# Kernel optimization log

Hardware: AMD Instinct MI355X
Metric: run time of the kernel (lower is better)

Reference implementation:

```python
import jax, jax.numpy as jnp
import numpy as np

B, S, D, H = 4, 2048, 768, 12
DEPTH = D // H


def setup_inputs() -> dict:
    key = jax.random.key(0)
    ks = jax.random.split(key, 8)
    scale = 1.0 / np.sqrt(D)
    inp = {
        "q": jax.random.normal(ks[0], (B, S, D), jnp.float32),
        "k": jax.random.normal(ks[1], (B, S, D), jnp.float32),
        "v": jax.random.normal(ks[2], (B, S, D), jnp.float32),
        # additive mask: 1.0 at disallowed (future) positions, causal
        "mask": jnp.triu(jnp.ones((S, S), jnp.float32), k=1)[None, None, :, :],
        "wq": jax.random.normal(ks[3], (D, D), jnp.float32) * scale,
        "wk": jax.random.normal(ks[4], (D, D), jnp.float32) * scale,
        "wv": jax.random.normal(ks[5], (D, D), jnp.float32) * scale,
        "w_dense": jax.random.normal(ks[6], (D, D), jnp.float32) * scale,
        "b_dense": jnp.zeros((D,), jnp.float32),
    }
    return inp


def _split_heads(x):
    b, s, _ = x.shape
    return x.reshape(b, s, H, DEPTH).transpose(0, 2, 1, 3)  # [B,H,S,depth]


def reference(q, k, v, mask, wq, wk, wv, w_dense, b_dense):
    qh = _split_heads(q @ wq.T)
    kh = _split_heads(k @ wk.T)
    vh = _split_heads(v @ wv.T)
    scale = jnp.sqrt(jnp.float32(DEPTH))
    logits = jnp.einsum("bhqd,bhkd->bhqk", qh, kh) / scale  # [B,H,S,S]
    logits = logits + mask * -1e9
    attn = jax.nn.softmax(logits, axis=-1)
    out = jnp.einsum("bhqk,bhkd->bhqd", attn, vh)
    out = out.transpose(0, 2, 1, 3).reshape(q.shape[0], -1, D)
    return out @ w_dense.T + b_dense
```

## Files before the change

### kernel.cpp

```cpp
#include <hip/hip_runtime.h>

typedef __attribute__((ext_vector_type(8))) short short8;
typedef __attribute__((ext_vector_type(4))) float f32x4;
typedef __attribute__((ext_vector_type(4))) unsigned int uint4v;

static __device__ __forceinline__ unsigned pack2(float x, float y) {
  unsigned ux = __float_as_uint(x) + 0x8000u;
  unsigned uy = __float_as_uint(y) + 0x8000u;
  return __builtin_amdgcn_perm(uy, ux, 0x07060302u);
}
static __device__ __forceinline__ unsigned packt(float x, float y) {
  return __builtin_amdgcn_perm(__float_as_uint(y), __float_as_uint(x), 0x07060302u);
}

#define GLDS(g, l)                                                                     \
  __builtin_amdgcn_global_load_lds((const __attribute__((address_space(1))) void*)(g), \
                                   (__attribute__((address_space(3))) void*)(l), 16, 0, 0)

__global__ __launch_bounds__(256) void cvt_all(const float* __restrict__ q,
                                               const float* __restrict__ k,
                                               const float* __restrict__ v,
                                               const float* __restrict__ w0,
                                               const float* __restrict__ w1,
                                               const float* __restrict__ w2,
                                               const float* __restrict__ w3,
                                               unsigned short* __restrict__ oq,
                                               unsigned short* __restrict__ ok,
                                               unsigned short* __restrict__ ov,
                                               unsigned short* __restrict__ o0,
                                               unsigned short* __restrict__ o1,
                                               unsigned short* __restrict__ o2,
                                               unsigned short* __restrict__ o3) {
  const int bx = blockIdx.x;
  const float* s;
  unsigned short* d;
  long i;
  if (bx < 18432) {
    int seg = bx / 6144;
    s = seg == 0 ? q : seg == 1 ? k : v;
    d = seg == 0 ? oq : seg == 1 ? ok : ov;
    i = (long)(bx - seg * 6144) * 256 + threadIdx.x;
  } else {
    int t = bx - 18432;
    int seg = t / 576;
    s = seg == 0 ? w0 : seg == 1 ? w1 : seg == 2 ? w2 : w3;
    d = seg == 0 ? o0 : seg == 1 ? o1 : seg == 2 ? o2 : o3;
    i = (long)(t - seg * 576) * 256 + threadIdx.x;
  }
  float4 val = ((const float4*)s)[i];
  uint2 o;
  o.x = pack2(val.x, val.y);
  o.y = pack2(val.z, val.w);
  *(uint2*)(d + 4 * i) = o;
}

template <int MODE>
static __device__ __forceinline__ void proj_body(const unsigned short* __restrict__ A,
                                                 const unsigned short* __restrict__ W,
                                                 unsigned short* __restrict__ O, int m0,
                                                 int n0, unsigned short* buf) {
  constexpr int K = 768;
  const int tid = threadIdx.x, lane = tid & 63, wave = tid >> 6;
  const int ln = lane & 15, quad = lane >> 4;
  const int wm = (wave & 1) << 6, wn = (wave >> 1) << 6;

  const int o0 = tid << 4, o1 = 4096 + (tid << 4);
  const unsigned short* gA0 = A + (long)(m0 + (o0 >> 6)) * K + ((o0 >> 4) & 3) * 8;
  const unsigned short* gA1 = A + (long)(m0 + (o1 >> 6)) * K + ((o1 >> 4) & 3) * 8;
  const unsigned short* gW0 = W + (long)(n0 + (o0 >> 6)) * K + ((o0 >> 4) & 3) * 8;
  const unsigned short* gW1 = W + (long)(n0 + (o1 >> 6)) * K + ((o1 >> 4) & 3) * 8;

  GLDS(gA0, buf + (o0 >> 1));
  GLDS(gA1, buf + (o1 >> 1));
  GLDS(gW0, buf + 8192 + (o0 >> 1));
  GLDS(gW1, buf + 8192 + (o1 >> 1));

  f32x4 acc[4][4] = {};
  for (int t = 0; t < 24; t++) {
    const int cur = t & 1, nxt = cur ^ 1;
    const int k1 = (t + 1) << 5;
    __syncthreads();
    if (t < 23) {
      GLDS(gA0 + k1, buf + nxt * 4096 + (o0 >> 1));
      GLDS(gA1 + k1, buf + nxt * 4096 + (o1 >> 1));
      GLDS(gW0 + k1, buf + 8192 + nxt * 4096 + (o0 >> 1));
      GLDS(gW1 + k1, buf + 8192 + nxt * 4096 + (o1 >> 1));
    }
    const unsigned short* As = buf + cur * 4096;
    const unsigned short* Bs = buf + 8192 + cur * 4096;
    short8 af[4], bfr[4];
#pragma unroll
    for (int mi = 0; mi < 4; mi++)
      af[mi] = *(const short8*)(As + (wm + mi * 16 + ln) * 32 + quad * 8);
#pragma unroll
    for (int ni = 0; ni < 4; ni++)
      bfr[ni] = *(const short8*)(Bs + (wn + ni * 16 + ln) * 32 + quad * 8);
#pragma unroll
    for (int mi = 0; mi < 4; mi++)
#pragma unroll
      for (int ni = 0; ni < 4; ni++)
        acc[mi][ni] = (MODE == 0)
                          ? __builtin_amdgcn_mfma_f32_16x16x32_bf16(bfr[ni], af[mi],
                                                                    acc[mi][ni], 0, 0, 0)
                          : __builtin_amdgcn_mfma_f32_16x16x32_bf16(af[mi], bfr[ni],
                                                                    acc[mi][ni], 0, 0, 0);
  }

  unsigned short* Ts = buf;
  __syncthreads();
  if (MODE == 0) {
#pragma unroll
    for (int mi = 0; mi < 4; mi++)
#pragma unroll
      for (int ni = 0; ni < 4; ni++) {
        f32x4 v = acc[mi][ni];
        int s = wm + mi * 16 + ln;
        int n = wn + ni * 16 + quad * 4;
        uint2 w2;
        w2.x = pack2(v[0], v[1]);
        w2.y = pack2(v[2], v[3]);
        *(uint2*)(Ts + s * 136 + n) = w2;
      }
    __syncthreads();
    const int part = tid & 7, sg0 = tid >> 3;
#pragma unroll
    for (int p = 0; p < 8; p++) {
      int seg = sg0 + p * 32;
      int hh = seg >> 7, s = seg & 127;
      short8 val = *(const short8*)(Ts + s * 136 + hh * 64 + part * 8);
      int gs = m0 + s;
      int bb = gs >> 11, srow = gs & 2047;
      int head = (n0 >> 6) + hh;
      *(short8*)(O + (((long)(bb * 12 + head) * 2048 + srow) << 6) + part * 8) = val;
    }
  } else {
#pragma unroll
    for (int mi = 0; mi < 4; mi++)
#pragma unroll
      for (int ni = 0; ni < 4; ni++) {
        f32x4 v = acc[mi][ni];
        int d = wn + ni * 16 + ln;
        int s = wm + mi * 16 + quad * 4;
        uint2 w2;
        w2.x = pack2(v[0], v[1]);
        w2.y = pack2(v[2], v[3]);
        *(uint2*)(Ts + d * 136 + s) = w2;
      }
    __syncthreads();
    const int part = tid & 15, r0 = tid >> 4;
    const int bb = m0 >> 11, sbase = m0 & 2047;
#pragma unroll
    for (int p = 0; p < 8; p++) {
      int d = r0 + p * 16;
      short8 val = *(const short8*)(Ts + d * 136 + part * 8);
      int head = (n0 >> 6) + (d >> 6);
      int dl = d & 63;
      *(short8*)(O + ((long)(bb * 12 + head) * 64 + dl) * 2048 + sbase + part * 8) = val;
    }
  }
}

__global__ __launch_bounds__(256) void proj_all(
    const unsigned short* __restrict__ qb, const unsigned short* __restrict__ kb,
    const unsigned short* __restrict__ vb, const unsigned short* __restrict__ wq,
    const unsigned short* __restrict__ wk, const unsigned short* __restrict__ wv,
    unsigned short* __restrict__ qh, unsigned short* __restrict__ kh,
    unsigned short* __restrict__ vt) {
  __shared__ unsigned short buf[17408];
  const int bx = blockIdx.x;
  const int xcd = bx & 7;
  const int i = bx >> 3;
  const int op = i / 48, j = i % 48;
  const int m0 = ((j / 6) * 8 + xcd) << 7, n0 = (j % 6) << 7;
  if (op == 0)
    proj_body<0>(qb, wq, qh, m0, n0, buf);
  else if (op == 1)
    proj_body<0>(kb, wk, kh, m0, n0, buf);
  else
    proj_body<1>(vb, wv, vt, m0, n0, buf);
}

__global__ __launch_bounds__(256) void dense_gemm(const unsigned short* __restrict__ A,
                                                  const unsigned short* __restrict__ W,
                                                  const float* __restrict__ bias,
                                                  float* __restrict__ out) {
  constexpr int K = 768;
  __shared__ unsigned short buf[16384];
  const int bx = blockIdx.x;
  const int xcd = bx & 7;
  const int i = bx >> 3;
  const int m0 = ((i / 6) * 8 + xcd) << 7;
  const int n0 = (i % 6) << 7;

  const int tid = threadIdx.x, lane = tid & 63, wave = tid >> 6;
  const int ln = lane & 15, quad = lane >> 4;
  const int wm = (wave & 1) << 6, wn = (wave >> 1) << 6;

  const int o0 = tid << 4, o1 = 4096 + (tid << 4);
  const unsigned short* gA0 = A + (long)(m0 + (o0 >> 6)) * K + ((o0 >> 4) & 3) * 8;
  const unsigned short* gA1 = A + (long)(m0 + (o1 >> 6)) * K + ((o1 >> 4) & 3) * 8;
  const unsigned short* gW0 = W + (long)(n0 + (o0 >> 6)) * K + ((o0 >> 4) & 3) * 8;
  const unsigned short* gW1 = W + (long)(n0 + (o1 >> 6)) * K + ((o1 >> 4) & 3) * 8;

  GLDS(gA0, buf + (o0 >> 1));
  GLDS(gA1, buf + (o1 >> 1));
  GLDS(gW0, buf + 8192 + (o0 >> 1));
  GLDS(gW1, buf + 8192 + (o1 >> 1));

  f32x4 acc[4][4] = {};
  for (int t = 0; t < 24; t++) {
    const int cur = t & 1, nxt = cur ^ 1;
    const int k1 = (t + 1) << 5;
    __syncthreads();
    if (t < 23) {
      GLDS(gA0 + k1, buf + nxt * 4096 + (o0 >> 1));
      GLDS(gA1 + k1, buf + nxt * 4096 + (o1 >> 1));
      GLDS(gW0 + k1, buf + 8192 + nxt * 4096 + (o0 >> 1));
      GLDS(gW1 + k1, buf + 8192 + nxt * 4096 + (o1 >> 1));
    }
    const unsigned short* As = buf + cur * 4096;
    const unsigned short* Bs = buf + 8192 + cur * 4096;
    short8 af[4], bfr[4];
#pragma unroll
    for (int mi = 0; mi < 4; mi++)
      af[mi] = *(const short8*)(As + (wm + mi * 16 + ln) * 32 + quad * 8);
#pragma unroll
    for (int ni = 0; ni < 4; ni++)
      bfr[ni] = *(const short8*)(Bs + (wn + ni * 16 + ln) * 32 + quad * 8);
#pragma unroll
    for (int mi = 0; mi < 4; mi++)
#pragma unroll
      for (int ni = 0; ni < 4; ni++)
        acc[mi][ni] =
            __builtin_amdgcn_mfma_f32_16x16x32_bf16(bfr[ni], af[mi], acc[mi][ni], 0, 0, 0);
  }

#pragma unroll
  for (int mi = 0; mi < 4; mi++) {
    const int m = m0 + wm + mi * 16 + ln;
#pragma unroll
    for (int ni = 0; ni < 4; ni++) {
      const int n = n0 + wn + ni * 16 + quad * 4;
      f32x4 v = acc[mi][ni];
      float4 bv = *(const float4*)(bias + n);
      float4 st;
      st.x = v[0] + bv.x;
      st.y = v[1] + bv.y;
      st.z = v[2] + bv.z;
      st.w = v[3] + bv.w;
      *(float4*)(out + (long)m * 768 + n) = st;
    }
  }
}

__global__ __launch_bounds__(256, 3) void attn_kernel(const unsigned short* __restrict__ Qh,
                                                      const unsigned short* __restrict__ Kh,
                                                      const unsigned short* __restrict__ Vt,
                                                      unsigned short* __restrict__ outp) {
  constexpr int S = 2048;
  constexpr float CEXP = 0.18033688011112042f;
  __shared__ unsigned short sbuf[16384];

  const int bx = blockIdx.x;
  const int xcd = bx & 7;
  const int ii = bx >> 3;
  const int pr = ii & 15, grp = ii >> 4;
  const int bh = grp * 8 + xcd;
  const int h = bh % 12, b = bh / 12;
  const int qtA = pr, qtB = 31 - pr;
  const int tid = threadIdx.x, wave = tid >> 6, lane = tid & 63;
  const int ln = lane & 15, quad = lane >> 4;

  const unsigned short* Qg = Qh + (long)(b * 12 + h) * S * 64;
  const unsigned short* Kg = Kh + (long)(b * 12 + h) * S * 64;
  const unsigned short* Vg = Vt + (long)(b * 12 + h) * 64 * S;

  const int qrA = qtA * 64 + wave * 16 + ln;
  const int qrB = qtB * 64 + wave * 16 + ln;

  short8 bQa0 = *(const short8*)(Qg + qrA * 64 + quad * 8);
  short8 bQa1 = *(const short8*)(Qg + qrA * 64 + 32 + quad * 8);
  short8 bQb0 = *(const short8*)(Qg + qrB * 64 + quad * 8);
  short8 bQb1 = *(const short8*)(Qg + qrB * 64 + 32 + quad * 8);

  float sumA = 0.f, sumB = 0.f;
  f32x4 Oa[4] = {};
  f32x4 Ob[4] = {};
  unsigned pkA[8][2], pkB[8][2];

  const int nkA = (qtA >> 1) + 1;
  const int nkB = (qtB >> 1) + 1;
  const int l0 = ln + ((quad & 1) << 5);
  const bool hi = quad >= 2;

  const int srow = tid >> 2, sc = (tid & 3) << 3;
  const int koff0 = srow * 64 + sc;
  const int koff1 = (srow + 64) * 64 + sc;
  const int koff2 = srow * 64 + 32 + sc;
  const int koff3 = (srow + 64) * 64 + 32 + sc;
  const long voff = (long)srow * 2048 + sc;

  short8 kc[4], vc[4];
  {
    kc[0] = *(const short8*)(Kg + koff0);
    kc[1] = *(const short8*)(Kg + koff1);
    kc[2] = *(const short8*)(Kg + koff2);
    kc[3] = *(const short8*)(Kg + koff3);
    vc[0] = *(const short8*)(Vg + voff);
    vc[1] = *(const short8*)(Vg + voff + 32);
    vc[2] = *(const short8*)(Vg + voff + 64);
    vc[3] = *(const short8*)(Vg + voff + 96);
  }

  for (int kt = 0; kt < nkB; kt++) {
    __syncthreads();
    {
      unsigned short* w = sbuf + tid * 8;
      *(short8*)(w) = kc[0];
      *(short8*)(w + 2048) = kc[1];
      *(short8*)(w + 4096) = kc[2];
      *(short8*)(w + 6144) = kc[3];
      *(short8*)(w + 8192) = vc[0];
      *(short8*)(w + 10240) = vc[1];
      *(short8*)(w + 12288) = vc[2];
      *(short8*)(w + 14336) = vc[3];
    }
    __syncthreads();
    if (kt + 1 < nkB) {
      const unsigned short* kg = Kg + (kt + 1) * 8192;
      const unsigned short* vg = Vg + (kt + 1) * 128;
      kc[0] = *(const short8*)(kg + koff0);
      kc[1] = *(const short8*)(kg + koff1);
      kc[2] = *(const short8*)(kg + koff2);
      kc[3] = *(const short8*)(kg + koff3);
      vc[0] = *(const short8*)(vg + voff);
      vc[1] = *(const short8*)(vg + voff + 32);
      vc[2] = *(const short8*)(vg + voff + 64);
      vc[3] = *(const short8*)(vg + voff + 96);
    }

    const bool actA = kt < nkA;
    const bool dgA = actA && (kt == nkA - 1);
    const bool dgB = (kt == nkB - 1);
    const int limA = actA ? (dgA ? ((qtA & 1) ? 8 : 4) : 8) : 0;
    const int limB = dgB ? ((qtB & 1) ? 8 : 4) : 8;
    const int limQ = limA > limB ? limA : limB;
    const int kbase = kt * 128 + quad * 4;

#pragma unroll
    for (int ni = 0; ni < 8; ni++) {
      if (ni < limQ) {
        const int fro = (ni * 16 + ln) * 32 + quad * 8;
        short8 k0 = *(const short8*)(sbuf + fro);
        short8 k1 = *(const short8*)(sbuf + 4096 + fro);
        const int key = kbase + ni * 16;
        if (ni < limA) {
          f32x4 s = {};
          s = __builtin_amdgcn_mfma_f32_16x16x32_bf16(k0, bQa0, s, 0, 0, 0);
          s = __builtin_amdgcn_mfma_f32_16x16x32_bf16(k1, bQa1, s, 0, 0, 0);
          float p0 = exp2f(s[0] * CEXP), p1 = exp2f(s[1] * CEXP);
          float p2 = exp2f(s[2] * CEXP), p3 = exp2f(s[3] * CEXP);
          if (dgA) {
            p0 = (key + 0 > qrA) ? 0.f : p0;
            p1 = (key + 1 > qrA) ? 0.f : p1;
            p2 = (key + 2 > qrA) ? 0.f : p2;
            p3 = (key + 3 > qrA) ? 0.f : p3;
          }
          sumA += (p0 + p1) + (p2 + p3);
          pkA[ni][0] = packt(p0, p1);
          pkA[ni][1] = packt(p2, p3);
        }
        if (ni < limB) {
          f32x4 s = {};
          s = __builtin_amdgcn_mfma_f32_16x16x32_bf16(k0, bQb0, s, 0, 0, 0);
          s = __builtin_amdgcn_mfma_f32_16x16x32_bf16(k1, bQb1, s, 0, 0, 0);
          float p0 = exp2f(s[0] * CEXP), p1 = exp2f(s[1] * CEXP);
          float p2 = exp2f(s[2] * CEXP), p3 = exp2f(s[3] * CEXP);
          if (dgB) {
            p0 = (key + 0 > qrB) ? 0.f : p0;
            p1 = (key + 1 > qrB) ? 0.f : p1;
            p2 = (key + 2 > qrB) ? 0.f : p2;
            p3 = (key + 3 > qrB) ? 0.f : p3;
          }
          sumB += (p0 + p1) + (p2 + p3);
          pkB[ni][0] = packt(p0, p1);
          pkB[ni][1] = packt(p2, p3);
        }
      }
    }

    auto mkB = [&](unsigned (&pk)[8][2], int kk) -> short8 {
      unsigned va0 = (unsigned)__shfl((int)pk[2 * kk][0], l0, 64);
      unsigned vb0 = (unsigned)__shfl((int)pk[2 * kk + 1][0], l0, 64);
      unsigned va1 = (unsigned)__shfl((int)pk[2 * kk][1], l0, 64);
      unsigned vb1 = (unsigned)__shfl((int)pk[2 * kk + 1][1], l0, 64);
      unsigned va2 = (unsigned)__shfl((int)pk[2 * kk][0], l0 + 16, 64);
      unsigned vb2 = (unsigned)__shfl((int)pk[2 * kk + 1][0], l0 + 16, 64);
      unsigned va3 = (unsigned)__shfl((int)pk[2 * kk][1], l0 + 16, 64);
      unsigned vb3 = (unsigned)__shfl((int)pk[2 * kk + 1][1], l0 + 16, 64);
      uint4v tv;
      tv.x = hi ? vb0 : va0;
      tv.y = hi ? vb1 : va1;
      tv.z = hi ? vb2 : va2;
      tv.w = hi ? vb3 : va3;
      return __builtin_bit_cast(short8, tv);
    };

    const int kkA = limA >> 1, kkB = limB >> 1;
#pragma unroll
    for (int kk = 0; kk < 4; kk++) {
      if (kk < kkB) {
        short8 Bb = mkB(pkB, kk);
        short8 Ba;
        if (kk < kkA) Ba = mkB(pkA, kk);
        const unsigned short* vp = sbuf + 8192 + kk * 2048;
#pragma unroll
        for (int di = 0; di < 4; di++) {
          short8 aV = *(const short8*)(vp + (di * 16 + ln) * 32 + quad * 8);
          Ob[di] = __builtin_amdgcn_mfma_f32_16x16x32_bf16(aV, Bb, Ob[di], 0, 0, 0);
          if (kk < kkA) Oa[di] = __builtin_amdgcn_mfma_f32_16x16x32_bf16(aV, Ba, Oa[di], 0, 0, 0);
        }
      }
    }
  }

  sumA += __shfl_xor(sumA, 16);
  sumA += __shfl_xor(sumA, 32);
  sumB += __shfl_xor(sumB, 16);
  sumB += __shfl_xor(sumB, 32);

  __syncthreads();
  unsigned short* Ts = sbuf;
  {
    float rlA = 1.0f / sumA, rlB = 1.0f / sumB;
    const int row = wave * 16 + ln;
#pragma unroll
    for (int di = 0; di < 4; di++) {
      uint2 wa, wb;
      wa.x = pack2(Oa[di][0] * rlA, Oa[di][1] * rlA);
      wa.y = pack2(Oa[di][2] * rlA, Oa[di][3] * rlA);
      wb.x = pack2(Ob[di][0] * rlB, Ob[di][1] * rlB);
      wb.y = pack2(Ob[di][2] * rlB, Ob[di][3] * rlB);
      *(uint2*)(Ts + row * 72 + di * 16 + quad * 4) = wa;
      *(uint2*)(Ts + (row + 64) * 72 + di * 16 + quad * 4) = wb;
    }
  }
  __syncthreads();
  const int part = tid & 7, r0 = tid >> 3;
#pragma unroll
  for (int p = 0; p < 4; p++) {
    int row = r0 + p * 32;
    int seg = row >> 6, qq = row & 63;
    int qrow = (seg ? qtB : qtA) * 64 + qq;
    short8 val = *(const short8*)(Ts + row * 72 + part * 8);
    *(short8*)(outp + ((long)b * S + qrow) * 768 + h * 64 + part * 8) = val;
  }
}

extern "C" void kernel_launch(void* const* d_in, const int* in_sizes, int n_in,
                              void* d_out, int out_size, void* d_ws, size_t ws_size,
                              hipStream_t stream) {
  const float* q = (const float*)d_in[0];
  const float* k = (const float*)d_in[1];
  const float* v = (const float*)d_in[2];
  const float* wq = (const float*)d_in[4];
  const float* wk = (const float*)d_in[5];
  const float* wv = (const float*)d_in[6];
  const float* wd = (const float*)d_in[7];
  const float* bd = (const float*)d_in[8];
  float* out = (float*)d_out;

  const long QKV = 4L * 2048 * 768;
  const long WN = 768L * 768;
  if (ws_size < (size_t)(7 * QKV + 4 * WN) * 2) return;

  unsigned short* qb = (unsigned short*)d_ws;
  unsigned short* kb = qb + QKV;
  unsigned short* vb = kb + QKV;
  unsigned short* wqb = vb + QKV;
  unsigned short* wkb = wqb + WN;
  unsigned short* wvb = wkb + WN;
  unsigned short* wdb = wvb + WN;
  unsigned short* qh = wdb + WN;
  unsigned short* kh = qh + QKV;
  unsigned short* vt = kh + QKV;
  unsigned short* at = vt + QKV;

  cvt_all<<<20736, 256, 0, stream>>>(q, k, v, wq, wk, wv, wd, qb, kb, vb, wqb, wkb, wvb, wdb);
  proj_all<<<1152, 256, 0, stream>>>(qb, kb, vb, wqb, wkb, wvb, qh, kh, vt);
  attn_kernel<<<768, 256, 0, stream>>>(qh, kh, vt, at);
  dense_gemm<<<384, 256, 0, stream>>>(at, wdb, bd, out);
}
```

Baseline: 272.7 us.

## Swizzle LDS tile layout to avoid bank conflicts and fold softmax scale into Q projection

Applies an XOR swizzle to the 16-byte chunk column in LDS for the projection GEMM, dense GEMM and attention K/V tiles. Both the global-to-LDS write addresses and the MFMA fragment read addresses are permuted so that lanes reading adjacent rows hit different banks. The log2e/sqrt(depth) softmax scale is also multiplied into Q when the projection is stored, which removes a multiply per logit in the attention inner loop. The cost is extra index arithmetic and one bf16 rounding of the pre-scaled Q values.

```diff
diff --git a/kernel.cpp b/kernel.cpp
--- a/kernel.cpp
+++ b/kernel.cpp
@@ -58,22 +58,26 @@
 static __device__ __forceinline__ void proj_body(const unsigned short* __restrict__ A,
                                                  const unsigned short* __restrict__ W,
                                                  unsigned short* __restrict__ O, int m0,
-                                                 int n0, unsigned short* buf) {
+                                                 int n0, unsigned short* buf,
+                                                 float scale) {
   constexpr int K = 768;
   const int tid = threadIdx.x, lane = tid & 63, wave = tid >> 6;
   const int ln = lane & 15, quad = lane >> 4;
   const int wm = (wave & 1) << 6, wn = (wave >> 1) << 6;
 
   const int o0 = tid << 4, o1 = 4096 + (tid << 4);
-  const unsigned short* gA0 = A + (long)(m0 + (o0 >> 6)) * K + ((o0 >> 4) & 3) * 8;
-  const unsigned short* gA1 = A + (long)(m0 + (o1 >> 6)) * K + ((o1 >> 4) & 3) * 8;
-  const unsigned short* gW0 = W + (long)(n0 + (o0 >> 6)) * K + ((o0 >> 4) & 3) * 8;
-  const unsigned short* gW1 = W + (long)(n0 + (o1 >> 6)) * K + ((o1 >> 4) & 3) * 8;
+  const int cxp = (((tid & 3) ^ ((tid >> 3) & 3)) << 3);
+  const unsigned short* gA0 = A + (long)(m0 + (o0 >> 6)) * K + cxp;
+  const unsigned short* gA1 = A + (long)(m0 + (o1 >> 6)) * K + cxp;
+  const unsigned short* gW0 = W + (long)(n0 + (o0 >> 6)) * K + cxp;
+  const unsigned short* gW1 = W + (long)(n0 + (o1 >> 6)) * K + cxp;
 
   GLDS(gA0, buf + (o0 >> 1));
   GLDS(gA1, buf + (o1 >> 1));
   GLDS(gW0, buf + 8192 + (o0 >> 1));
   GLDS(gW1, buf + 8192 + (o1 >> 1));
+
+  const int qsw = (quad * 8) ^ (((ln >> 1) & 3) << 3);
 
   f32x4 acc[4][4] = {};
   for (int t = 0; t < 24; t++) {
@@ -91,10 +95,10 @@
     short8 af[4], bfr[4];
 #pragma unroll
     for (int mi = 0; mi < 4; mi++)
-      af[mi] = *(const short8*)(As + (wm + mi * 16 + ln) * 32 + quad * 8);
+      af[mi] = *(const short8*)(As + (wm + mi * 16 + ln) * 32 + qsw);
 #pragma unroll
     for (int ni = 0; ni < 4; ni++)
-      bfr[ni] = *(const short8*)(Bs + (wn + ni * 16 + ln) * 32 + quad * 8);
+      bfr[ni] = *(const short8*)(Bs + (wn + ni * 16 + ln) * 32 + qsw);
 #pragma unroll
     for (int mi = 0; mi < 4; mi++)
 #pragma unroll
@@ -117,8 +121,8 @@
         int s = wm + mi * 16 + ln;
         int n = wn + ni * 16 + quad * 4;
         uint2 w2;
-        w2.x = pack2(v[0], v[1]);
-        w2.y = pack2(v[2], v[3]);
+        w2.x = pack2(v[0] * scale, v[1] * scale);
+        w2.y = pack2(v[2] * scale, v[3] * scale);
         *(uint2*)(Ts + s * 136 + n) = w2;
       }
     __syncthreads();
@@ -173,11 +177,11 @@
   const int op = i / 48, j = i % 48;
   const int m0 = ((j / 6) * 8 + xcd) << 7, n0 = (j % 6) << 7;
   if (op == 0)
-    proj_body<0>(qb, wq, qh, m0, n0, buf);
+    proj_body<0>(qb, wq, qh, m0, n0, buf, 0.18033688011112042f);
   else if (op == 1)
-    proj_body<0>(kb, wk, kh, m0, n0, buf);
+    proj_body<0>(kb, wk, kh, m0, n0, buf, 1.0f);
   else
-    proj_body<1>(vb, wv, vt, m0, n0, buf);
+    proj_body<1>(vb, wv, vt, m0, n0, buf, 1.0f);
 }
 
 __global__ __launch_bounds__(256) void dense_gemm(const unsigned short* __restrict__ A,
@@ -197,15 +201,18 @@
   const int wm = (wave & 1) << 6, wn = (wave >> 1) << 6;
 
   const int o0 = tid << 4, o1 = 4096 + (tid << 4);
-  const unsigned short* gA0 = A + (long)(m0 + (o0 >> 6)) * K + ((o0 >> 4) & 3) * 8;
-  const unsigned short* gA1 = A + (long)(m0 + (o1 >> 6)) * K + ((o1 >> 4) & 3) * 8;
-  const unsigned short* gW0 = W + (long)(n0 + (o0 >> 6)) * K + ((o0 >> 4) & 3) * 8;
-  const unsigned short* gW1 = W + (long)(n0 + (o1 >> 6)) * K + ((o1 >> 4) & 3) * 8;
+  const int cxp = (((tid & 3) ^ ((tid >> 3) & 3)) << 3);
+  const unsigned short* gA0 = A + (long)(m0 + (o0 >> 6)) * K + cxp;
+  const unsigned short* gA1 = A + (long)(m0 + (o1 >> 6)) * K + cxp;
+  const unsigned short* gW0 = W + (long)(n0 + (o0 >> 6)) * K + cxp;
+  const unsigned short* gW1 = W + (long)(n0 + (o1 >> 6)) * K + cxp;
 
   GLDS(gA0, buf + (o0 >> 1));
   GLDS(gA1, buf + (o1 >> 1));
   GLDS(gW0, buf + 8192 + (o0 >> 1));
   GLDS(gW1, buf + 8192 + (o1 >> 1));
+
+  const int qsw = (quad * 8) ^ (((ln >> 1) & 3) << 3);
 
   f32x4 acc[4][4] = {};
   for (int t = 0; t < 24; t++) {
@@ -223,10 +230,10 @@
     short8 af[4], bfr[4];
 #pragma unroll
     for (int mi = 0; mi < 4; mi++)
-      af[mi] = *(const short8*)(As + (wm + mi * 16 + ln) * 32 + quad * 8);
+      af[mi] = *(const short8*)(As + (wm + mi * 16 + ln) * 32 + qsw);
 #pragma unroll
     for (int ni = 0; ni < 4; ni++)
-      bfr[ni] = *(const short8*)(Bs + (wn + ni * 16 + ln) * 32 + quad * 8);
+      bfr[ni] = *(const short8*)(Bs + (wn + ni * 16 + ln) * 32 + qsw);
 #pragma unroll
     for (int mi = 0; mi < 4; mi++)
 #pragma unroll
@@ -258,7 +265,6 @@
                                                       const unsigned short* __restrict__ Vt,
                                                       unsigned short* __restrict__ outp) {
   constexpr int S = 2048;
-  constexpr float CEXP = 0.18033688011112042f;
   __shared__ unsigned short sbuf[16384];
 
   const int bx = blockIdx.x;
@@ -299,6 +305,9 @@
   const int koff2 = srow * 64 + 32 + sc;
   const int koff3 = (srow + 64) * 64 + 32 + sc;
   const long voff = (long)srow * 2048 + sc;
+
+  const int wsw = (tid * 8) ^ (((tid >> 3) & 3) << 3);
+  const int qsw = (quad * 8) ^ (((ln >> 1) & 3) << 3);
 
   short8 kc[4], vc[4];
   {
@@ -315,7 +324,7 @@
   for (int kt = 0; kt < nkB; kt++) {
     __syncthreads();
     {
-      unsigned short* w = sbuf + tid * 8;
+      unsigned short* w = sbuf + wsw;
       *(short8*)(w) = kc[0];
       *(short8*)(w + 2048) = kc[1];
       *(short8*)(w + 4096) = kc[2];
@@ -350,7 +359,7 @@
 #pragma unroll
     for (int ni = 0; ni < 8; ni++) {
       if (ni < limQ) {
-        const int fro = (ni * 16 + ln) * 32 + quad * 8;
+        const int fro = (ni * 16 + ln) * 32 + qsw;
         short8 k0 = *(const short8*)(sbuf + fro);
         short8 k1 = *(const short8*)(sbuf + 4096 + fro);
         const int key = kbase + ni * 16;
@@ -358,8 +367,8 @@
           f32x4 s = {};
           s = __builtin_amdgcn_mfma_f32_16x16x32_bf16(k0, bQa0, s, 0, 0, 0);
           s = __builtin_amdgcn_mfma_f32_16x16x32_bf16(k1, bQa1, s, 0, 0, 0);
-          float p0 = exp2f(s[0] * CEXP), p1 = exp2f(s[1] * CEXP);
-          float p2 = exp2f(s[2] * CEXP), p3 = exp2f(s[3] * CEXP);
+          float p0 = exp2f(s[0]), p1 = exp2f(s[1]);
+          float p2 = exp2f(s[2]), p3 = exp2f(s[3]);
           if (dgA) {
             p0 = (key + 0 > qrA) ? 0.f : p0;
             p1 = (key + 1 > qrA) ? 0.f : p1;
@@ -374,8 +383,8 @@
           f32x4 s = {};
           s = __builtin_amdgcn_mfma_f32_16x16x32_bf16(k0, bQb0, s, 0, 0, 0);
           s = __builtin_amdgcn_mfma_f32_16x16x32_bf16(k1, bQb1, s, 0, 0, 0);
-          float p0 = exp2f(s[0] * CEXP), p1 = exp2f(s[1] * CEXP);
-          float p2 = exp2f(s[2] * CEXP), p3 = exp2f(s[3] * CEXP);
+          float p0 = exp2f(s[0]), p1 = exp2f(s[1]);
+          float p2 = exp2f(s[2]), p3 = exp2f(s[3]);
           if (dgB) {
             p0 = (key + 0 > qrB) ? 0.f : p0;
             p1 = (key + 1 > qrB) ? 0.f : p1;
@@ -416,7 +425,7 @@
         const unsigned short* vp = sbuf + 8192 + kk * 2048;
 #pragma unroll
         for (int di = 0; di < 4; di++) {
-          short8 aV = *(const short8*)(vp + (di * 16 + ln) * 32 + quad * 8);
+          short8 aV = *(const short8*)(vp + (di * 16 + ln) * 32 + qsw);
           Ob[di] = __builtin_amdgcn_mfma_f32_16x16x32_bf16(aV, Bb, Ob[di], 0, 0, 0);
           if (kk < kkA) Oa[di] = __builtin_amdgcn_mfma_f32_16x16x32_bf16(aV, Ba, Oa[di], 0, 0, 0);
         }
```

Result: no change. 269.2 us (-1.3%).
